# Optimization experiments

Measured on AMD Instinct MI355X. Metric: run time of the kernel, lower is better.

## Reference

```python
import jax, jax.numpy as jnp
import numpy as np

C = 1.0                 # ball curvature magnitude (k = -c)
SQRT_C = float(np.sqrt(C))
MIN_NORM = 1e-15
BALL_EPS = 4e-3         # geoopt float32 projection eps


def _artanh(x):
    return jnp.arctanh(jnp.clip(x, -1.0 + 1e-7, 1.0 - 1e-7))


def _norm(x):
    return jnp.clip(jnp.linalg.norm(x, axis=-1, keepdims=True), MIN_NORM)


def expmap0(u):
    n = _norm(u)
    return jnp.tanh(SQRT_C * n) * u / (SQRT_C * n)


def logmap0(y):
    n = _norm(y)
    return _artanh(SQRT_C * n) * y / (SQRT_C * n)


def mobius_add(x, y):
    x2 = jnp.sum(x * x, axis=-1, keepdims=True)
    y2 = jnp.sum(y * y, axis=-1, keepdims=True)
    xy = jnp.sum(x * y, axis=-1, keepdims=True)
    num = (1.0 + 2.0 * C * xy + C * y2) * x + (1.0 - C * x2) * y
    den = 1.0 + 2.0 * C * xy + C * C * x2 * y2
    return num / jnp.clip(den, MIN_NORM)


def mobius_matvec(W, x):
    # x: [N, in], W: [out, in]
    mx = x @ W.T                                   # [N, out]
    xn = _norm(x)
    mxn = _norm(mx)
    res = jnp.tanh(mxn / xn * _artanh(SQRT_C * xn)) * mx / (mxn * SQRT_C)
    zero = jnp.linalg.norm(mx, axis=-1, keepdims=True) <= 1e-10
    return jnp.where(zero, jnp.zeros_like(res), res)


def project(x):
    n = _norm(x)
    maxnorm = (1.0 - BALL_EPS) / SQRT_C
    return jnp.where(n > maxnorm, x * (maxnorm / n), x)


def setup_inputs() -> dict:
    key = jax.random.key(0)
    k1, k2, k3, k4, k5 = jax.random.split(key, 5)
    N, E, D_IN, D_OUT = 100000, 600000, 128, 128
    x_h = jax.random.normal(k1, (N, D_IN), dtype=jnp.float32) * 0.05  # inside ball
    edge_index = jax.random.randint(k2, (2, E), 0, N, dtype=jnp.int64)
    edge_weight = jax.random.uniform(k3, (E,), dtype=jnp.float32)
    xav = float(np.sqrt(2.0 / (D_IN + D_OUT)))
    W = jax.random.normal(k4, (D_OUT, D_IN), dtype=jnp.float32) * xav
    b = jax.random.normal(k5, (D_OUT,), dtype=jnp.float32) * 0.01
    a = jnp.asarray(0.25, dtype=jnp.float32)  # PReLU slope
    return {"x_h": x_h, "edge_index": edge_index, "edge_weight": edge_weight,
            "W": W, "b": b, "a": a}


def reference(x_h, edge_index, edge_weight, W, b, a):
    N = x_h.shape[0]
    # HyperbolicLinear: mobius matvec + mobius bias add
    h = mobius_matvec(W, x_h)
    h = mobius_add(h, expmap0(b))
    # tangent-space aggregation
    h_t = logmap0(h)                                  # [N, D]
    src, dst = edge_index[0], edge_index[1]
    msg = h_t[src] * edge_weight[:, None]             # [E, D]
    agg = jax.ops.segment_sum(msg, dst, num_segments=N) + h_t
    # mobius PReLU activation
    h2_t = logmap0(expmap0(agg))
    h2_t = jnp.where(h2_t >= 0, h2_t, a * h2_t)
    return project(expmap0(h2_t))
```

## Files before the change

### kernel.cpp

```cpp
#include <hip/hip_runtime.h>
#include <hip/hip_fp16.h>
#include <cstdint>

#define D 128
#define BLK 256

constexpr float MINN    = 1e-15f;
constexpr float ATCLIP  = 1.0f - 1e-7f;
constexpr float BALLEPS = 4e-3f;

typedef _Float16 f16x8 __attribute__((ext_vector_type(8)));
typedef float    f32x4 __attribute__((ext_vector_type(4)));

union H4 { _Float16 h[4]; uint2 u2; };
union H8 { _Float16 h[8]; uint4 u4; };

typedef __attribute__((address_space(1))) const void gas_v;
typedef __attribute__((address_space(3))) void las_v;

__device__ __forceinline__ float red64(float v) {
    v += __shfl_xor(v, 1, 64);
    v += __shfl_xor(v, 2, 64);
    v += __shfl_xor(v, 4, 64);
    v += __shfl_xor(v, 8, 64);
    v += __shfl_xor(v, 16, 64);
    v += __shfl_xor(v, 32, 64);
    return v;
}

__device__ __forceinline__ int red64i(int v) {
    v += __shfl_xor(v, 1, 64);
    v += __shfl_xor(v, 2, 64);
    v += __shfl_xor(v, 4, 64);
    v += __shfl_xor(v, 8, 64);
    v += __shfl_xor(v, 16, 64);
    v += __shfl_xor(v, 32, 64);
    return v;
}

__device__ __forceinline__ float red16(float v) {
    v += __shfl_xor(v, 1, 64);
    v += __shfl_xor(v, 2, 64);
    v += __shfl_xor(v, 4, 64);
    v += __shfl_xor(v, 8, 64);
    return v;
}

__device__ __forceinline__ float tanh_fast(float x) {
    float e = __expf(2.f * fminf(x, 15.f));
    return __fdividef(e - 1.f, e + 1.f);
}
__device__ __forceinline__ float artanh_fast(float x) {
    x = fminf(x, ATCLIP);
    return 0.5f * __logf(__fdividef(1.f + x, 1.f - x));
}

__global__ __launch_bounds__(256) void k_prep(const float* __restrict__ W,
                                              _Float16* __restrict__ Wh,
                                              int* __restrict__ zero, int zeroInts)
{
    const int t = threadIdx.x;
    const int bid = blockIdx.x;
    if (bid < 8) {
        int i = bid * 256 + t;
        int f = i >> 7;
        int r = i & 127;
        const float4* src = (const float4*)(W + r * 128 + f * 8);
        float4 v0 = src[0], v1 = src[1];
        H8 u;
        u.h[0] = (_Float16)v0.x; u.h[1] = (_Float16)v0.y;
        u.h[2] = (_Float16)v0.z; u.h[3] = (_Float16)v0.w;
        u.h[4] = (_Float16)v1.x; u.h[5] = (_Float16)v1.y;
        u.h[6] = (_Float16)v1.z; u.h[7] = (_Float16)v1.w;
        *(uint4*)(Wh + i * 8) = u.u4;
    } else {
        int i = (bid - 8) * 256 + t;
        int base = i * 4;
        if (base + 3 < zeroInts) {
            *(int4*)(zero + base) = make_int4(0, 0, 0, 0);
        } else if (base < zeroInts) {
            for (int k = base; k < zeroInts; ++k) zero[k] = 0;
        }
    }
}

__global__ __launch_bounds__(256) void k_hist(const int* __restrict__ ei,
                                              int* __restrict__ cnt,
                                              int* __restrict__ rank,
                                              int E, int use_rank)
{
    const int* dsts = ei + E;
    int i0 = (blockIdx.x * 256 + threadIdx.x) * 4;
    if (((E & 3) == 0) && (i0 + 4 <= E)) {
        int4 d = *(const int4*)(dsts + i0);
        int r0 = atomicAdd(&cnt[d.x], 1);
        int r1 = atomicAdd(&cnt[d.y], 1);
        int r2 = atomicAdd(&cnt[d.z], 1);
        int r3 = atomicAdd(&cnt[d.w], 1);
        if (use_rank) *(int4*)(rank + i0) = make_int4(r0, r1, r2, r3);
    } else {
        for (int e = i0; e < E && e < i0 + 4; ++e) {
            int r = atomicAdd(&cnt[dsts[e]], 1);
            if (use_rank) rank[e] = r;
        }
    }
}

__global__ __launch_bounds__(BLK) void k_node_mfma(
    const float* __restrict__ x, const _Float16* __restrict__ Wh,
    const float* __restrict__ b, uint2* __restrict__ ht, int N)
{
    __shared__ float xs[64 * 128];

    const int t     = threadIdx.x;
    const int lane  = t & 63;
    const int w     = t >> 6;
    const int node0 = blockIdx.x * 128;

    float2 b2 = ((const float2*)b)[lane];
    __builtin_amdgcn_sched_barrier(0);

#pragma unroll
    for (int i = 0; i < 8; ++i) {
        int P      = (w * 8 + i) * 64 + lane;
        int node   = P >> 5;
        int q      = (P & 31) ^ (node & 7);
        int node_g = min(node0 + node, N - 1);
        const float* src = x + (size_t)node_g * 128 + q * 4;
        char* dst = (char*)xs + (size_t)(w * 8 + i) * 1024;
        __builtin_amdgcn_global_load_lds((gas_v*)src, (las_v*)dst, 16, 0, 0);
    }
    __builtin_amdgcn_sched_barrier(0);

    f32x4 rv[8];
#pragma unroll
    for (int i = 0; i < 8; ++i) {
        int P      = (w * 8 + i) * 64 + lane;
        int node   = P >> 5;
        int q      = (P & 31) ^ (node & 7);
        int node_g = min(node0 + 64 + node, N - 1);
        rv[i] = *(const f32x4*)(x + (size_t)node_g * 128 + q * 4);
    }
    __builtin_amdgcn_sched_barrier(0);

    float pb  = fmaf(b2.x, b2.x, b2.y * b2.y);
    float bn2 = red64(pb);
    float bnc    = fmaxf(sqrtf(bn2), MINN);
    float bscale = __fdividef(tanh_fast(bnc), bnc);
    const float y2 = bscale * bscale * bn2;

    const int c = lane & 15;
    const int g = lane >> 4;
    const int bnode = w * 16 + c;
    const int sw    = bnode & 7;
    const float* xrow = &xs[bnode * 128];
    const float4* b4  = (const float4*)b;
    uint2* lout = (uint2*)((char*)xs + (size_t)w * 8192);

    auto do_tile = [&](int tb) {
        f32x4 Cf[8];
#pragma unroll
        for (int mt = 0; mt < 8; ++mt) Cf[mt] = (f32x4){0.f, 0.f, 0.f, 0.f};
        float px = 0.f;

#pragma unroll
        for (int s = 0; s < 4; ++s) {
            int q0 = s * 8 + g * 2;
            f32x4 lo = *(const f32x4*)&xrow[(q0 ^ sw) * 4];
            f32x4 hi = *(const f32x4*)&xrow[((q0 + 1) ^ sw) * 4];
            px = fmaf(lo[0], lo[0], px); px = fmaf(lo[1], lo[1], px);
            px = fmaf(lo[2], lo[2], px); px = fmaf(lo[3], lo[3], px);
            px = fmaf(hi[0], hi[0], px); px = fmaf(hi[1], hi[1], px);
            px = fmaf(hi[2], hi[2], px); px = fmaf(hi[3], hi[3], px);
            f16x8 Bf;
            Bf[0] = (_Float16)lo[0]; Bf[1] = (_Float16)lo[1];
            Bf[2] = (_Float16)lo[2]; Bf[3] = (_Float16)lo[3];
            Bf[4] = (_Float16)hi[0]; Bf[5] = (_Float16)hi[1];
            Bf[6] = (_Float16)hi[2]; Bf[7] = (_Float16)hi[3];
            const _Float16* wp = Wh + ((s * 4 + g) << 10) + (c << 3);
#pragma unroll
            for (int mt = 0; mt < 8; ++mt) {
                f16x8 Af = *(const f16x8*)&wp[mt << 7];
                Cf[mt] = __builtin_amdgcn_mfma_f32_16x16x32_f16(Af, Bf, Cf[mt], 0, 0, 0);
            }
        }

        float pm = 0.f, pdb = 0.f;
#pragma unroll
        for (int mt = 0; mt < 8; ++mt) {
            float4 bv = b4[mt * 4 + g];
            pm  = fmaf(Cf[mt][0], Cf[mt][0], pm);
            pm  = fmaf(Cf[mt][1], Cf[mt][1], pm);
            pm  = fmaf(Cf[mt][2], Cf[mt][2], pm);
            pm  = fmaf(Cf[mt][3], Cf[mt][3], pm);
            pdb = fmaf(Cf[mt][0], bv.x, pdb);
            pdb = fmaf(Cf[mt][1], bv.y, pdb);
            pdb = fmaf(Cf[mt][2], bv.z, pdb);
            pdb = fmaf(Cf[mt][3], bv.w, pdb);
        }
        float xn2 = px;
        xn2 += __shfl_xor(xn2, 16); xn2 += __shfl_xor(xn2, 32);
        pm  += __shfl_xor(pm, 16);  pm  += __shfl_xor(pm, 32);
        pdb += __shfl_xor(pdb, 16); pdb += __shfl_xor(pdb, 32);
        float pd = bscale * pdb;

        float xn      = fmaxf(sqrtf(xn2), MINN);
        float mxn_raw = sqrtf(pm);
        float mxn     = fmaxf(mxn_raw, MINN);
        float alpha   = __fdividef(tanh_fast(__fdividef(mxn, xn) * artanh_fast(xn)), mxn);
        if (mxn_raw <= 1e-10f) alpha = 0.f;

        float x2  = alpha * alpha * pm;
        float xy  = alpha * pd;
        float den = fmaxf(fmaf(x2, y2, 1.f + 2.f * xy), MINN);
        float ca  = __fdividef((1.f + 2.f * xy + y2) * alpha, den);
        float cb  = __fdividef(1.f - x2, den);

        float hn2 = ca * ca * pm + 2.f * ca * cb * pd + cb * cb * y2;
        float hn  = fmaxf(sqrtf(hn2), MINN);
        float lsc = __fdividef(artanh_fast(hn), hn);
        float s1  = lsc * ca;
        float s2b = lsc * cb * bscale;

#pragma unroll
        for (int mt = 0; mt < 8; ++mt) {
            float4 bv = b4[mt * 4 + g];
            H4 u;
            u.h[0] = (_Float16)fmaf(s1, Cf[mt][0], s2b * bv.x);
            u.h[1] = (_Float16)fmaf(s1, Cf[mt][1], s2b * bv.y);
            u.h[2] = (_Float16)fmaf(s1, Cf[mt][2], s2b * bv.z);
            u.h[3] = (_Float16)fmaf(s1, Cf[mt][3], s2b * bv.w);
            lout[c * 33 + mt * 4 + g] = u.u2;
        }
    };

    auto copyout = [&](int tb) {
#pragma unroll
        for (int it = 0; it < 8; ++it) {
            int lin  = it * BLK + t;
            int node = lin >> 5;
            int col  = lin & 31;
            int gn   = tb + node;
            if (gn < N) {
                const uint2* lsrc = (const uint2*)((const char*)xs + (size_t)(node >> 4) * 8192);
                ht[(size_t)gn * 32 + col] = lsrc[(node & 15) * 33 + col];
            }
        }
    };

    asm volatile("s_waitcnt vmcnt(8)" ::: "memory");
    __builtin_amdgcn_sched_barrier(0);

    do_tile(node0);
    __syncthreads();
    copyout(node0);

    asm volatile("s_waitcnt lgkmcnt(0)" ::: "memory");
    __builtin_amdgcn_sched_barrier(0);
    __builtin_amdgcn_s_barrier();
    __builtin_amdgcn_sched_barrier(0);

#pragma unroll
    for (int i = 0; i < 8; ++i) {
        float* dst = (float*)((char*)xs + (size_t)(w * 8 + i) * 1024 + (size_t)lane * 16);
        *(f32x4*)dst = rv[i];
    }

    do_tile(node0 + 64);
    __syncthreads();
    copyout(node0 + 64);
}

__global__ __launch_bounds__(256) void k_scan(
    const int* __restrict__ cnt, int* __restrict__ ptr,
    unsigned long long* __restrict__ lb, int N)
{
    __shared__ int s[256];
    __shared__ int sbase;
    const int t   = threadIdx.x;
    const int bid = blockIdx.x;
    const int lane = t & 63;
    const int w    = t >> 6;

    int base = bid * 1024 + t * 4;
    int v0 = 0, v1 = 0, v2 = 0, v3 = 0;
    if (base + 3 < N) {
        int4 q = *(const int4*)&cnt[base];
        v0 = q.x; v1 = q.y; v2 = q.z; v3 = q.w;
    } else {
        if (base + 0 < N) v0 = cnt[base + 0];
        if (base + 1 < N) v1 = cnt[base + 1];
        if (base + 2 < N) v2 = cnt[base + 2];
        if (base + 3 < N) v3 = cnt[base + 3];
    }
    int sum = v0 + v1 + v2 + v3;
    s[t] = sum;
    __syncthreads();
    for (int off = 1; off < 256; off <<= 1) {
        int xv = (t >= off) ? s[t - off] : 0;
        __syncthreads();
        s[t] += xv;
        __syncthreads();
    }
    int excl  = s[t] - sum;
    int total = s[255];

    if (t == 255) {
        unsigned long long pkt =
            ((unsigned long long)((bid == 0) ? 2u : 1u) << 32) | (unsigned)total;
        __hip_atomic_store(&lb[bid], pkt, __ATOMIC_RELEASE, __HIP_MEMORY_SCOPE_AGENT);
        if (bid == 0) sbase = 0;
    }

    if (bid > 0 && w == 3) {
        int exclb = 0;
        int j = bid - 1;
        while (true) {
            int idx = j - lane;
            unsigned f = 0; int v = 0;
            if (idx >= 0) {
                unsigned long long p;
                do {
                    p = __hip_atomic_load(&lb[idx], __ATOMIC_ACQUIRE, __HIP_MEMORY_SCOPE_AGENT);
                    f = (unsigned)(p >> 32);
                } while (f == 0);
                v = (int)(unsigned)(p & 0xffffffffu);
            }
            unsigned long long m2 = __ballot(f == 2u);
            if (m2) {
                int Lstop = __ffsll((long long)m2) - 1;
                int contrib = (lane <= Lstop) ? v : 0;
                exclb += red64i(contrib);
                break;
            } else {
                exclb += red64i((idx >= 0) ? v : 0);
                j -= 64;
            }
        }
        if (lane == 0) {
            unsigned long long pkt2 =
                ((unsigned long long)2u << 32) | (unsigned)(exclb + total);
            __hip_atomic_store(&lb[bid], pkt2, __ATOMIC_RELEASE, __HIP_MEMORY_SCOPE_AGENT);
            sbase = exclb;
        }
    }
    __syncthreads();

    int r = excl + sbase;
    if (base + 0 < N) ptr[base + 0] = r; r += v0;
    if (base + 1 < N) ptr[base + 1] = r; r += v1;
    if (base + 2 < N) ptr[base + 2] = r; r += v2;
    if (base + 3 < N) ptr[base + 3] = r;
}

__global__ __launch_bounds__(256) void k_scatter_rank(
    const int* __restrict__ ei, const float* __restrict__ ew,
    const int* __restrict__ ptr, const int* __restrict__ rank,
    int2* __restrict__ sorted, int E)
{
    int e = blockIdx.x * 256 + threadIdx.x;
    if (e >= E) return;
    int src = ei[e];
    int dst = ei[E + e];
    float w = ew[e];
    int pos = ptr[dst] + rank[e];
    sorted[pos] = make_int2(src << 8, __float_as_int(w));
}

__global__ __launch_bounds__(256) void k_scatter_atomic(
    const int* __restrict__ ei, const float* __restrict__ ew,
    int* __restrict__ ptr, int2* __restrict__ sorted, int E)
{
    int e = blockIdx.x * 256 + threadIdx.x;
    if (e >= E) return;
    int src = ei[e];
    int dst = ei[E + e];
    float w = ew[e];
    int pos = atomicAdd(&ptr[dst], 1);
    sorted[pos] = make_int2(src << 8, __float_as_int(w));
}

__global__ __launch_bounds__(256) void k_agg_final(
    const char* __restrict__ htb, const int* __restrict__ ptr,
    const int* __restrict__ cnt, const int2* __restrict__ sorted,
    const float* __restrict__ a_in, float* __restrict__ out, int N, int rmode)
{
    const int t   = threadIdx.x;
    const int li  = t & 15;
    const int grp = t >> 4;
    const int n   = blockIdx.x * 16 + grp;
    if (n >= N) return;
    const float a = a_in[0];

    H8 own; own.u4 = *(const uint4*)(htb + (size_t)n * 256 + li * 16);
    float acc[8];
#pragma unroll
    for (int k = 0; k < 8; ++k) acc[k] = (float)own.h[k];

    int basep = ptr[n];
    int cn    = cnt[n];
    int s0    = rmode ? basep : basep - cn;
    int e0    = s0 + cn;

    const int lioff = li * 16;
    int j = s0;
    for (; j + 4 <= e0; j += 4) {
        int2 d0 = sorted[j];
        int2 d1 = sorted[j + 1];
        int2 d2 = sorted[j + 2];
        int2 d3 = sorted[j + 3];
        H8 g0, g1, g2, g3;
        g0.u4 = *(const uint4*)(htb + (unsigned)d0.x + lioff);
        g1.u4 = *(const uint4*)(htb + (unsigned)d1.x + lioff);
        g2.u4 = *(const uint4*)(htb + (unsigned)d2.x + lioff);
        g3.u4 = *(const uint4*)(htb + (unsigned)d3.x + lioff);
        float w0 = __int_as_float(d0.y);
        float w1 = __int_as_float(d1.y);
        float w2 = __int_as_float(d2.y);
        float w3 = __int_as_float(d3.y);
#pragma unroll
        for (int k = 0; k < 8; ++k) acc[k] = fmaf((float)g0.h[k], w0, acc[k]);
#pragma unroll
        for (int k = 0; k < 8; ++k) acc[k] = fmaf((float)g1.h[k], w1, acc[k]);
#pragma unroll
        for (int k = 0; k < 8; ++k) acc[k] = fmaf((float)g2.h[k], w2, acc[k]);
#pragma unroll
        for (int k = 0; k < 8; ++k) acc[k] = fmaf((float)g3.h[k], w3, acc[k]);
    }
    for (; j < e0; ++j) {
        int2 d = sorted[j];
        H8 g; g.u4 = *(const uint4*)(htb + (unsigned)d.x + lioff);
        float w = __int_as_float(d.y);
#pragma unroll
        for (int k = 0; k < 8; ++k) acc[k] = fmaf((float)g.h[k], w, acc[k]);
    }

    float pv = 0.f;
#pragma unroll
    for (int k = 0; k < 8; ++k) {
        float v = acc[k];
        v = (v >= 0.f) ? v : a * v;
        acc[k] = v;
        pv = fmaf(v, v, pv);
    }
    float m2 = red16(pv);
    float rc = fmaxf(sqrtf(m2), MINN);
    float te = tanh_fast(rc);
    const float maxn = 1.0f - BALLEPS;
    float fsc = __fdividef(fminf(fmaxf(te, MINN), maxn), rc);

    float4 o0 = make_float4(fsc * acc[0], fsc * acc[1], fsc * acc[2], fsc * acc[3]);
    float4 o1 = make_float4(fsc * acc[4], fsc * acc[5], fsc * acc[6], fsc * acc[7]);
    float4* orow = (float4*)(out + (size_t)n * D);
    orow[li * 2 + 0] = o0;
    orow[li * 2 + 1] = o1;
}

extern "C" void kernel_launch(void* const* d_in, const int* in_sizes, int n_in,
                              void* d_out, int out_size, void* d_ws, size_t ws_size,
                              hipStream_t stream)
{
    const float* x  = (const float*)d_in[0];
    const int*   ei = (const int*)  d_in[1];
    const float* ew = (const float*)d_in[2];
    const float* W  = (const float*)d_in[3];
    const float* b  = (const float*)d_in[4];
    const float* a  = (const float*)d_in[5];
    float* out = (float*)d_out;

    const int N = in_sizes[0] / D;
    const int E = in_sizes[1] / 2;
    const int nc = (N + 1023) / 1024;

    char* ws = (char*)d_ws;
    size_t HT_B       = (size_t)N * D * 2;
    uint2*              ht  = (uint2*)ws;
    size_t off_cnt    = HT_B;
    int*                cnt = (int*)(ws + off_cnt);
    size_t off_lb     = (off_cnt + (size_t)N * 4 + 15) & ~(size_t)15;
    unsigned long long* lb  = (unsigned long long*)(ws + off_lb);
    size_t off_ptr    = (off_lb + (size_t)nc * 8 + 15) & ~(size_t)15;
    int*                ptr = (int*)(ws + off_ptr);
    size_t off_sorted = (off_ptr + (size_t)N * 4 + 15) & ~(size_t)15;
    int2*               sorted = (int2*)(ws + off_sorted);
    size_t off_wh     = off_sorted + (size_t)E * 8;
    _Float16*           Wh  = (_Float16*)(ws + off_wh);
    size_t off_rank   = off_wh + 32768;
    int*                rank = (int*)(ws + off_rank);
    int use_rank = (ws_size >= off_rank + (size_t)E * 4) ? 1 : 0;

    int zeroInts = (int)((off_ptr - off_cnt) / 4);
    int zb  = ((zeroInts + 3) / 4 + 255) / 256;
    int nb1 = (N + 127) / 128;
    int hb  = (E + 1023) / 1024;

    k_prep<<<8 + zb, 256, 0, stream>>>(W, Wh, cnt, zeroInts);
    k_hist<<<hb, 256, 0, stream>>>(ei, cnt, use_rank ? rank : cnt, E, use_rank);
    k_node_mfma<<<nb1, BLK, 0, stream>>>(x, Wh, b, ht, N);
    k_scan<<<nc, 256, 0, stream>>>(cnt, ptr, lb, N);
    if (use_rank)
        k_scatter_rank<<<(E + 255) / 256, 256, 0, stream>>>(ei, ew, ptr, rank, sorted, E);
    else
        k_scatter_atomic<<<(E + 255) / 256, 256, 0, stream>>>(ei, ew, ptr, sorted, E);
    k_agg_final<<<(N + 15) / 16, 256, 0, stream>>>((const char*)ht, ptr, cnt, sorted, a, out, N, use_rank);
}
```

Before: 212.0 us.

## Fuse destination histogram into node MFMA kernel to overlap atomics with compute

Removes the separate histogram kernel and gives each node-transform block a slice of edges. The block loads its destination indices up front and issues the count atomics after its tiles are computed. The goal is to drop one launch and hide the atomic traffic behind the matmul work, at the cost of extra registers and a longer tail in each block.

```diff
diff --git a/kernel.cpp b/kernel.cpp
--- a/kernel.cpp
+++ b/kernel.cpp
@@ -84,31 +84,11 @@
     }
 }
 
-__global__ __launch_bounds__(256) void k_hist(const int* __restrict__ ei,
-                                              int* __restrict__ cnt,
-                                              int* __restrict__ rank,
-                                              int E, int use_rank)
-{
-    const int* dsts = ei + E;
-    int i0 = (blockIdx.x * 256 + threadIdx.x) * 4;
-    if (((E & 3) == 0) && (i0 + 4 <= E)) {
-        int4 d = *(const int4*)(dsts + i0);
-        int r0 = atomicAdd(&cnt[d.x], 1);
-        int r1 = atomicAdd(&cnt[d.y], 1);
-        int r2 = atomicAdd(&cnt[d.z], 1);
-        int r3 = atomicAdd(&cnt[d.w], 1);
-        if (use_rank) *(int4*)(rank + i0) = make_int4(r0, r1, r2, r3);
-    } else {
-        for (int e = i0; e < E && e < i0 + 4; ++e) {
-            int r = atomicAdd(&cnt[dsts[e]], 1);
-            if (use_rank) rank[e] = r;
-        }
-    }
-}
-
 __global__ __launch_bounds__(BLK) void k_node_mfma(
     const float* __restrict__ x, const _Float16* __restrict__ Wh,
-    const float* __restrict__ b, uint2* __restrict__ ht, int N)
+    const float* __restrict__ b, uint2* __restrict__ ht, int N,
+    const int* __restrict__ ei, int* __restrict__ cnt,
+    int* __restrict__ rank, int E, int eslice, int use_rank)
 {
     __shared__ float xs[64 * 128];
 
@@ -116,6 +96,15 @@
     const int lane  = t & 63;
     const int w     = t >> 6;
     const int node0 = blockIdx.x * 128;
+    const int e0    = blockIdx.x * eslice;
+
+    int ed[4];
+#pragma unroll
+    for (int k = 0; k < 4; ++k) {
+        int idx = min(e0 + k * BLK + t, E - 1);
+        ed[k] = ei[E + idx];
+    }
+    __builtin_amdgcn_sched_barrier(0);
 
     float2 b2 = ((const float2*)b)[lane];
     __builtin_amdgcn_sched_barrier(0);
@@ -269,6 +258,23 @@
     do_tile(node0 + 64);
     __syncthreads();
     copyout(node0 + 64);
+
+#pragma unroll
+    for (int k = 0; k < 4; ++k) {
+        int i = k * BLK + t;
+        int e = e0 + i;
+        if (i < eslice && e < E) {
+            int r = atomicAdd(&cnt[ed[k]], 1);
+            if (use_rank) rank[e] = r;
+        }
+    }
+    for (int i = 4 * BLK + t; i < eslice; i += BLK) {
+        int e = e0 + i;
+        if (e < E) {
+            int r = atomicAdd(&cnt[ei[E + e]], 1);
+            if (use_rank) rank[e] = r;
+        }
+    }
 }
 
 __global__ __launch_bounds__(256) void k_scan(
@@ -492,11 +498,11 @@
     int zeroInts = (int)((off_ptr - off_cnt) / 4);
     int zb  = ((zeroInts + 3) / 4 + 255) / 256;
     int nb1 = (N + 127) / 128;
-    int hb  = (E + 1023) / 1024;
+    int eslice = (E + nb1 - 1) / nb1;
 
     k_prep<<<8 + zb, 256, 0, stream>>>(W, Wh, cnt, zeroInts);
-    k_hist<<<hb, 256, 0, stream>>>(ei, cnt, use_rank ? rank : cnt, E, use_rank);
-    k_node_mfma<<<nb1, BLK, 0, stream>>>(x, Wh, b, ht, N);
+    k_node_mfma<<<nb1, BLK, 0, stream>>>(x, Wh, b, ht, N, ei, cnt,
+                                         use_rank ? rank : nullptr, E, eslice, use_rank);
     k_scan<<<nc, 256, 0, stream>>>(cnt, ptr, lb, N);
     if (use_rank)
         k_scatter_rank<<<(E + 255) / 256, 256, 0, stream>>>(ei, ew, ptr, rank, sorted, E);
```

New measurement: 204.0 us. 3.8% less time.
